# Performance work log

Measured on AMD Instinct MI355X. Metric: run time of the kernel, lower is better.

## Reference

```python
import jax, jax.numpy as jnp
import numpy as np

N = 100000       # num nodes
E = 3200000      # num edges (avg degree 32)
F_IN = 128       # num_node_features
HID = 16         # hidden dim hard-coded in Net
C = 10           # num_classes


def setup_inputs() -> dict:
    key = jax.random.key(0)
    k1, k2, k3, k4 = jax.random.split(key, 4)
    x = jax.random.normal(k1, (N, F_IN), dtype=jnp.float32)
    edge_index = jax.random.randint(k2, (2, E), 0, N, dtype=jnp.int32)
    W1 = jax.random.normal(k3, (F_IN, HID), dtype=jnp.float32) * 0.05
    b1 = jnp.zeros((HID,), dtype=jnp.float32)
    W2 = jax.random.normal(k4, (HID, C), dtype=jnp.float32) * 0.05
    b2 = jnp.zeros((C,), dtype=jnp.float32)
    return {"x": x, "edge_index": edge_index, "W1": W1, "b1": b1, "W2": W2, "b2": b2}


def reference(x, edge_index, W1, b1, W2, b2):
    # GCNConv: out = D^{-1/2} (A + I) D^{-1/2} X W + b   (add self-loops)
    loops = jnp.arange(N, dtype=edge_index.dtype)
    row = jnp.concatenate([edge_index[0], loops])  # source nodes
    col = jnp.concatenate([edge_index[1], loops])  # target nodes

    # symmetric normalization (degrees include self-loops, so deg >= 1)
    deg = jax.ops.segment_sum(jnp.ones_like(col, dtype=jnp.float32), col, num_segments=N)
    dis = jax.lax.rsqrt(deg)
    norm = dis[row] * dis[col]  # [E+N]

    def gcn_conv(h, W, b):
        h = h @ W                               # [N, d_out] small GEMM first
        msg = h[row] * norm[:, None]            # gather + scale, [E+N, d_out]
        out = jax.ops.segment_sum(msg, col, num_segments=N)  # scatter-add
        return out + b

    h = jax.nn.relu(gcn_conv(x, W1, b1))
    # F.dropout(training=False) is identity in eval mode
    logits = gcn_conv(h, W2, b2)
    return jax.nn.log_softmax(logits, axis=1)
```

## Files before the change

### kernel.cpp

```cpp
#include <hip/hip_runtime.h>
#include <math.h>

#define N_NODES 100000
#define N_EDGES 3200000
#define F_IN 128
#define HID 16
#define C_OUT 10
#define WIN 256
#define NDIG 391
#define PNB2 500
#define EPB 6400
#define SCN (NDIG * PNB2)
#define SB1 764
#define MAXE2 20
#define CSRLDS 10240

typedef unsigned short u16;
typedef unsigned int u32;

__device__ __forceinline__ float bf2f(u16 u) {
    return __uint_as_float(((u32)u) << 16);
}
__device__ __forceinline__ u16 f2bf(float f) {
    u32 x = __float_as_uint(f);
    u32 r = (x + 0x7fffu + ((x >> 16) & 1u)) >> 16;
    return (u16)r;
}
__device__ __forceinline__ void acc8(float* a, uint4 w) {
    a[0] += bf2f((u16)(w.x & 0xffff)); a[1] += bf2f((u16)(w.x >> 16));
    a[2] += bf2f((u16)(w.y & 0xffff)); a[3] += bf2f((u16)(w.y >> 16));
    a[4] += bf2f((u16)(w.z & 0xffff)); a[5] += bf2f((u16)(w.z >> 16));
    a[6] += bf2f((u16)(w.w & 0xffff)); a[7] += bf2f((u16)(w.w >> 16));
}

__global__ void k_pcnt(const int* __restrict__ col, int* __restrict__ blkhistA) {
    __shared__ int h[NDIG];
    for (int i = threadIdx.x; i < NDIG; i += 256) h[i] = 0;
    __syncthreads();
    const uint4* c4 = (const uint4*)(col + blockIdx.x * EPB);
    for (int i = threadIdx.x; i < EPB / 4; i += 256) {
        uint4 c = c4[i];
        atomicAdd(&h[c.x >> 8], 1);
        atomicAdd(&h[c.y >> 8], 1);
        atomicAdd(&h[c.z >> 8], 1);
        atomicAdd(&h[c.w >> 8], 1);
    }
    __syncthreads();
    for (int d = threadIdx.x; d < NDIG; d += 256)
        blkhistA[d * PNB2 + blockIdx.x] = h[d];
}

__global__ void k_s1(const int* __restrict__ blkhistA, int* __restrict__ psum) {
    __shared__ int sm[256];
    int i = blockIdx.x * 256 + threadIdx.x;
    sm[threadIdx.x] = (i < SCN) ? blkhistA[i] : 0;
    __syncthreads();
    for (int off = 128; off > 0; off >>= 1) {
        if (threadIdx.x < off) sm[threadIdx.x] += sm[threadIdx.x + off];
        __syncthreads();
    }
    if (threadIdx.x == 0) psum[blockIdx.x] = sm[0];
}

__global__ void k_s3(const int* __restrict__ blkhistA, const int* __restrict__ psum,
                     int* __restrict__ blkhistB) {
    __shared__ int ps[1024];
    __shared__ int sm[256];
    int t = threadIdx.x;
    for (int i = t; i < 1024; i += 256) ps[i] = (i < SB1) ? psum[i] : 0;
    __syncthreads();
    for (int off = 1; off < 1024; off <<= 1) {
        int v[4];
#pragma unroll
        for (int j = 0; j < 4; j++) {
            int idx = t + j * 256;
            v[j] = ps[idx] + ((idx >= off) ? ps[idx - off] : 0);
        }
        __syncthreads();
#pragma unroll
        for (int j = 0; j < 4; j++) ps[t + j * 256] = v[j];
        __syncthreads();
    }
    int bpre = (blockIdx.x > 0) ? ps[blockIdx.x - 1] : 0;

    int i = blockIdx.x * 256 + t;
    int v = (i < SCN) ? blkhistA[i] : 0;
    sm[t] = v;
    __syncthreads();
    for (int off = 1; off < 256; off <<= 1) {
        int a = sm[t];
        int b = (t >= off) ? sm[t - off] : 0;
        __syncthreads();
        sm[t] = a + b;
        __syncthreads();
    }
    if (i < SCN) blkhistB[i] = bpre + sm[t] - v;
}

__global__ void __launch_bounds__(512) k_pwrite(
        const int* __restrict__ row, const int* __restrict__ col,
        const int* __restrict__ blkhistA, const int* __restrict__ blkhistB,
        u32* __restrict__ staging) {
    __shared__ u32 sorted[EPB];
    __shared__ u16 dwin[EPB];
    __shared__ int gbase[NDIG];
    __shared__ int lbase[NDIG];
    __shared__ int lcur[NDIG];
    __shared__ int scan[512];

    int t = threadIdx.x;
    int b = blockIdx.x;
    int hv = 0;
    if (t < NDIG) {
        hv = blkhistA[t * PNB2 + b];
        gbase[t] = blkhistB[t * PNB2 + b];
        lcur[t] = 0;
    }
    scan[t] = hv;
    __syncthreads();
    for (int off = 1; off < 512; off <<= 1) {
        int v = scan[t];
        int u = (t >= off) ? scan[t - off] : 0;
        __syncthreads();
        scan[t] = v + u;
        __syncthreads();
    }
    if (t < NDIG) lbase[t] = scan[t] - hv;
    __syncthreads();

    const uint4* c4 = (const uint4*)(col + b * EPB);
    const uint4* r4 = (const uint4*)(row + b * EPB);
    for (int i = t; i < EPB / 4; i += 512) {
        uint4 c = c4[i];
        uint4 r = r4[i];
        int d, rank, pos;
        d = (int)(c.x >> 8); rank = atomicAdd(&lcur[d], 1); pos = lbase[d] + rank;
        sorted[pos] = ((c.x & 255u) << 17) | r.x; dwin[pos] = (u16)d;
        d = (int)(c.y >> 8); rank = atomicAdd(&lcur[d], 1); pos = lbase[d] + rank;
        sorted[pos] = ((c.y & 255u) << 17) | r.y; dwin[pos] = (u16)d;
        d = (int)(c.z >> 8); rank = atomicAdd(&lcur[d], 1); pos = lbase[d] + rank;
        sorted[pos] = ((c.z & 255u) << 17) | r.z; dwin[pos] = (u16)d;
        d = (int)(c.w >> 8); rank = atomicAdd(&lcur[d], 1); pos = lbase[d] + rank;
        sorted[pos] = ((c.w & 255u) << 17) | r.w; dwin[pos] = (u16)d;
    }
    __syncthreads();

    for (int i = t; i < EPB; i += 512) {
        int d = dwin[i];
        staging[gbase[d] + (i - lbase[d])] = sorted[i];
    }
}

__global__ void __launch_bounds__(512) k_csr(
        u32* staging, const int* __restrict__ blkhistB,
        int* __restrict__ offs, float* __restrict__ dis) {
    __shared__ u32 sorted[CSRLDS];
    __shared__ int cnt[WIN];
    __shared__ int base[WIN];
    int w = blockIdx.x;
    int t = threadIdx.x;
    if (t < WIN) cnt[t] = 0;
    __syncthreads();
    int start = blkhistB[w * PNB2];
    int end = (w == NDIG - 1) ? N_EDGES : blkhistB[(w + 1) * PNB2];
    int m = end - start;
    u32 buf[MAXE2];
    int n = 0;
#pragma unroll
    for (int k = 0; k < MAXE2; k++) {
        int i = k * 512 + t;
        if (i < m) {
            u32 e = staging[start + i];
            buf[k] = e;
            n = k + 1;
            atomicAdd(&cnt[e >> 17], 1);
        }
    }
    __syncthreads();
    if (t < WIN) base[t] = cnt[t];
    __syncthreads();
    for (int off = 1; off < WIN; off <<= 1) {
        int v = 0;
        if (t < WIN) {
            v = base[t];
            if (t >= off) v += base[t - off];
        }
        __syncthreads();
        if (t < WIN) base[t] = v;
        __syncthreads();
    }
    if (t < WIN) {
        int excl = base[t] - cnt[t];
        base[t] = excl;
        int node = w * WIN + t;
        if (node < N_NODES) {
            offs[node] = start + excl;
            dis[node] = rsqrtf(1.0f + (float)cnt[t]);
        }
    }
    if (w == 0 && t == 0) offs[N_NODES] = N_EDGES;
    __syncthreads();
#pragma unroll
    for (int k = 0; k < MAXE2; k++) {
        if (k < n) {
            u32 e = buf[k];
            int pos = atomicAdd(&base[(int)(e >> 17)], 1);
            sorted[pos] = e;
        }
    }
    __syncthreads();
    for (int i = t; i < m; i += 512)
        staging[start + i] = sorted[i];
}

__global__ void k_gemm1(const float* __restrict__ x, const float* __restrict__ W1,
                        const float* __restrict__ dis, u16* __restrict__ h1s) {
    __shared__ float Ws[F_IN * HID];
    for (int t = threadIdx.x; t < F_IN * HID; t += blockDim.x) Ws[t] = W1[t];
    __syncthreads();

    int node = blockIdx.x * blockDim.x + threadIdx.x;
    if (node >= N_NODES) return;

    float acc[HID];
#pragma unroll
    for (int j = 0; j < HID; j++) acc[j] = 0.f;

    const float4* xr = (const float4*)(x + (size_t)node * F_IN);
#pragma unroll 2
    for (int k4 = 0; k4 < F_IN / 4; k4++) {
        float4 v = xr[k4];
        float xv[4] = {v.x, v.y, v.z, v.w};
#pragma unroll
        for (int kk = 0; kk < 4; kk++) {
            const float4* wr = (const float4*)(Ws + (k4 * 4 + kk) * HID);
            float4 w0 = wr[0], w1 = wr[1], w2 = wr[2], w3 = wr[3];
            float xs = xv[kk];
            acc[0]  += xs * w0.x; acc[1]  += xs * w0.y; acc[2]  += xs * w0.z; acc[3]  += xs * w0.w;
            acc[4]  += xs * w1.x; acc[5]  += xs * w1.y; acc[6]  += xs * w1.z; acc[7]  += xs * w1.w;
            acc[8]  += xs * w2.x; acc[9]  += xs * w2.y; acc[10] += xs * w2.z; acc[11] += xs * w2.w;
            acc[12] += xs * w3.x; acc[13] += xs * w3.y; acc[14] += xs * w3.z; acc[15] += xs * w3.w;
        }
    }

    float d = dis[node];
    u32 p[8];
#pragma unroll
    for (int i = 0; i < 8; i++)
        p[i] = (u32)f2bf(acc[2 * i] * d) | ((u32)f2bf(acc[2 * i + 1] * d) << 16);
    u32* dst = (u32*)(h1s + (size_t)node * HID);
#pragma unroll
    for (int i = 0; i < 8; i++) dst[i] = p[i];
}

__global__ void k_gl1(const int* __restrict__ offs, const u32* __restrict__ csr,
                      const float* __restrict__ dis, const u16* __restrict__ h1s,
                      const float* __restrict__ b1, const float* __restrict__ W2,
                      u16* __restrict__ h2s) {
    __shared__ float Ws[HID * C_OUT];
    __shared__ float b1s[HID];
    if (threadIdx.x < HID * C_OUT) Ws[threadIdx.x] = W2[threadIdx.x];
    if (threadIdx.x < HID) b1s[threadIdx.x] = b1[threadIdx.x];
    __syncthreads();

    int t = blockIdx.x * 256 + threadIdx.x;
    if (t >= N_NODES * 8) return;
    int node = t >> 3;
    int q = t & 7;
    int half = q >> 2;
    int eq = q & 3;
    const uint4* hb = (const uint4*)h1s;
    float a[8] = {0.f, 0.f, 0.f, 0.f, 0.f, 0.f, 0.f, 0.f};
    if (eq == 0) acc8(a, hb[(size_t)node * 2 + half]);
    int o = offs[node + half];
    int oo = __shfl_xor(o, 4);
    int s0 = half ? oo : o;
    int s1 = half ? o : oo;
    int len = s1 - s0;
    int lo = s0 + ((len * eq) >> 2);
    int hi = s0 + ((len * (eq + 1)) >> 2);
    int j = lo;
    for (; j < hi && (j & 3); j++)
        acc8(a, hb[(size_t)(csr[j] & 0x1FFFFu) * 2 + half]);
    for (; j + 4 <= hi; j += 4) {
        uint4 ss = *(const uint4*)(csr + j);
        uint4 w0 = hb[(size_t)(ss.x & 0x1FFFFu) * 2 + half];
        uint4 w1 = hb[(size_t)(ss.y & 0x1FFFFu) * 2 + half];
        uint4 w2 = hb[(size_t)(ss.z & 0x1FFFFu) * 2 + half];
        uint4 w3 = hb[(size_t)(ss.w & 0x1FFFFu) * 2 + half];
        acc8(a, w0); acc8(a, w1); acc8(a, w2); acc8(a, w3);
    }
    for (; j < hi; j++)
        acc8(a, hb[(size_t)(csr[j] & 0x1FFFFu) * 2 + half]);

#pragma unroll
    for (int k = 0; k < 8; k++) {
        a[k] += __shfl_xor(a[k], 1);
        a[k] += __shfl_xor(a[k], 2);
    }

    float dc = dis[node];
    float own[8], oth[8];
#pragma unroll
    for (int k = 0; k < 8; k++) own[k] = a[k] * dc;
#pragma unroll
    for (int k = 0; k < 8; k++) oth[k] = __shfl_xor(own[k], 4);
    float h[16];
#pragma unroll
    for (int k = 0; k < 8; k++) {
        h[k]     = half ? oth[k] : own[k];
        h[8 + k] = half ? own[k] : oth[k];
    }
#pragma unroll
    for (int jj = 0; jj < 16; jj++) h[jj] = fmaxf(h[jj] + b1s[jj], 0.f);

    int nf = half ? 2 : 8;
    float outv[8];
#pragma unroll
    for (int k = 0; k < 8; k++) {
        float s = 0.f;
        if (k < nf) {
            int kk = half * 8 + k;
#pragma unroll
            for (int jj = 0; jj < 16; jj++) s += h[jj] * Ws[jj * C_OUT + kk];
        }
        outv[k] = s * dc;
    }
    if (eq == 0) {
        uint4 ov;
        ov.x = (u32)f2bf(outv[0]) | ((u32)f2bf(outv[1]) << 16);
        ov.y = half ? 0u : ((u32)f2bf(outv[2]) | ((u32)f2bf(outv[3]) << 16));
        ov.z = half ? 0u : ((u32)f2bf(outv[4]) | ((u32)f2bf(outv[5]) << 16));
        ov.w = half ? 0u : ((u32)f2bf(outv[6]) | ((u32)f2bf(outv[7]) << 16));
        ((uint4*)h2s)[(size_t)node * 2 + half] = ov;
    }
}

__global__ void k_gather2(const int* __restrict__ offs, const u32* __restrict__ csr,
                          const float* __restrict__ dis, const u16* __restrict__ h2s,
                          const float* __restrict__ b2, float* __restrict__ out) {
    __shared__ float b2s[C_OUT];
    if (threadIdx.x < C_OUT) b2s[threadIdx.x] = b2[threadIdx.x];
    __syncthreads();

    int t = blockIdx.x * 256 + threadIdx.x;
    if (t >= N_NODES * 8) return;
    int node = t >> 3;
    int q = t & 7;
    int half = q >> 2;
    int eq = q & 3;
    const uint4* hb = (const uint4*)h2s;
    float a[8] = {0.f, 0.f, 0.f, 0.f, 0.f, 0.f, 0.f, 0.f};
    if (eq == 0) acc8(a, hb[(size_t)node * 2 + half]);
    int o = offs[node + half];
    int oo = __shfl_xor(o, 4);
    int s0 = half ? oo : o;
    int s1 = half ? o : oo;
    int len = s1 - s0;
    int lo = s0 + ((len * eq) >> 2);
    int hi = s0 + ((len * (eq + 1)) >> 2);
    int j = lo;
    for (; j < hi && (j & 3); j++)
        acc8(a, hb[(size_t)(csr[j] & 0x1FFFFu) * 2 + half]);
    for (; j + 4 <= hi; j += 4) {
        uint4 ss = *(const uint4*)(csr + j);
        uint4 w0 = hb[(size_t)(ss.x & 0x1FFFFu) * 2 + half];
        uint4 w1 = hb[(size_t)(ss.y & 0x1FFFFu) * 2 + half];
        uint4 w2 = hb[(size_t)(ss.z & 0x1FFFFu) * 2 + half];
        uint4 w3 = hb[(size_t)(ss.w & 0x1FFFFu) * 2 + half];
        acc8(a, w0); acc8(a, w1); acc8(a, w2); acc8(a, w3);
    }
    for (; j < hi; j++)
        acc8(a, hb[(size_t)(csr[j] & 0x1FFFFu) * 2 + half]);

#pragma unroll
    for (int k = 0; k < 8; k++) {
        a[k] += __shfl_xor(a[k], 1);
        a[k] += __shfl_xor(a[k], 2);
    }

    float dc = dis[node];
    int nf = half ? 2 : 8;
    float lg[8];
    float m = -1e30f;
#pragma unroll
    for (int k = 0; k < 8; k++) {
        lg[k] = a[k] * dc + b2s[(half * 8 + k) % C_OUT];
        if (k < nf) m = fmaxf(m, lg[k]);
    }
    m = fmaxf(m, __shfl_xor(m, 4));
    float s = 0.f;
#pragma unroll
    for (int k = 0; k < 8; k++)
        if (k < nf) s += expf(lg[k] - m);
    s += __shfl_xor(s, 4);
    float ls = logf(s) + m;
    if (eq == 0) {
        float* dst = out + (size_t)node * C_OUT + half * 8;
        if (half == 0) {
#pragma unroll
            for (int i = 0; i < 4; i++)
                *(float2*)(dst + 2 * i) = make_float2(lg[2 * i] - ls, lg[2 * i + 1] - ls);
        } else {
            *(float2*)dst = make_float2(lg[0] - ls, lg[1] - ls);
        }
    }
}

extern "C" void kernel_launch(void* const* d_in, const int* in_sizes, int n_in,
                              void* d_out, int out_size, void* d_ws, size_t ws_size,
                              hipStream_t stream) {
    const float* x  = (const float*)d_in[0];
    const int*   ei = (const int*)d_in[1];
    const float* W1 = (const float*)d_in[2];
    const float* b1 = (const float*)d_in[3];
    const float* W2 = (const float*)d_in[4];
    const float* b2 = (const float*)d_in[5];
    float* out = (float*)d_out;

    const int* row = ei;
    const int* col = ei + N_EDGES;

    char* ws = (char*)d_ws;
    float* dis      = (float*)(ws);
    int*   offs     = (int*)(ws + 400000);
    int*   blkhistA = (int*)(ws + 800016);
    int*   blkhistB = (int*)(ws + 1582352);
    int*   psum     = (int*)(ws + 2364688);
    u32*   staging  = (u32*)(ws + 2367744);
    u16*   h1s      = (u16*)(ws + 15167744);
    u16*   h2s      = (u16*)(ws + 18367744);

    const int B = 256;
    int gN  = (N_NODES + B - 1) / B;
    int gN8 = (N_NODES * 8 + B - 1) / B;

    k_pcnt  <<<PNB2, B, 0, stream>>>(col, blkhistA);
    k_s1    <<<SB1, B, 0, stream>>>(blkhistA, psum);
    k_s3    <<<SB1, B, 0, stream>>>(blkhistA, psum, blkhistB);
    k_pwrite<<<PNB2, 512, 0, stream>>>(row, col, blkhistA, blkhistB, staging);
    k_csr   <<<NDIG, 512, 0, stream>>>(staging, blkhistB, offs, dis);
    k_gemm1 <<<gN, B, 0, stream>>>(x, W1, dis, h1s);
    k_gl1   <<<gN8, B, 0, stream>>>(offs, staging, dis, h1s, b1, W2, h2s);
    k_gather2<<<gN8, B, 0, stream>>>(offs, staging, dis, h2s, b2, out);
}
```

Baseline: 212.2 us.

## Sort nodes by degree within each window to balance gather warps

The CSR kernel now builds a per-window degree histogram and a counting sort that stores a permuted (node, degree) slot list plus per-slot edge start offsets. This replaces the offs array. Both gather kernels iterate over slots, so the threads in a wavefront handle nodes of similar degree, which should cut load imbalance and divergence. The gather inner loop is also unrolled to 8 edges to keep more loads in flight. Degree is stored in 8 bits and capped at 255, so the result would be wrong for any node with more than 255 in-edges.

```diff
diff --git a/kernel.cpp b/kernel.cpp
--- a/kernel.cpp
+++ b/kernel.cpp
@@ -14,6 +14,7 @@
 #define SB1 764
 #define MAXE2 20
 #define CSRLDS 10240
+#define NSLOT (NDIG * WIN)
 
 typedef unsigned short u16;
 typedef unsigned int u32;
@@ -153,13 +154,16 @@
 
 __global__ void __launch_bounds__(512) k_csr(
         u32* staging, const int* __restrict__ blkhistB,
-        int* __restrict__ offs, float* __restrict__ dis) {
+        u16* __restrict__ permdeg, int* __restrict__ starts, float* __restrict__ dis) {
     __shared__ u32 sorted[CSRLDS];
     __shared__ int cnt[WIN];
     __shared__ int base[WIN];
+    __shared__ int dh[256];
+    __shared__ int dsc[256];
     int w = blockIdx.x;
     int t = threadIdx.x;
     if (t < WIN) cnt[t] = 0;
+    if (t < 256) dh[t] = 0;
     __syncthreads();
     int start = blkhistB[w * PNB2];
     int end = (w == NDIG - 1) ? N_EDGES : blkhistB[(w + 1) * PNB2];
@@ -189,16 +193,44 @@
         if (t < WIN) base[t] = v;
         __syncthreads();
     }
+    int deg = 0, excl = 0;
+    int node = w * WIN + t;
     if (t < WIN) {
-        int excl = base[t] - cnt[t];
+        excl = base[t] - cnt[t];
         base[t] = excl;
-        int node = w * WIN + t;
+        deg = cnt[t];
         if (node < N_NODES) {
-            offs[node] = start + excl;
-            dis[node] = rsqrtf(1.0f + (float)cnt[t]);
-        }
-    }
-    if (w == 0 && t == 0) offs[N_NODES] = N_EDGES;
+            dis[node] = rsqrtf(1.0f + (float)deg);
+            atomicAdd(&dh[deg < 255 ? deg : 255], 1);
+        }
+    }
+    __syncthreads();
+    if (t < 256) dsc[t] = dh[t];
+    __syncthreads();
+    for (int off = 1; off < 256; off <<= 1) {
+        int v = 0;
+        if (t < 256) {
+            v = dsc[t];
+            if (t >= off) v += dsc[t - off];
+        }
+        __syncthreads();
+        if (t < 256) dsc[t] = v;
+        __syncthreads();
+    }
+    if (t < 256) dh[t] = dsc[t] - dh[t];
+    __syncthreads();
+    if (t < WIN) {
+        int rank, dcap = deg < 255 ? deg : 255;
+        if (node < N_NODES) {
+            rank = atomicAdd(&dh[dcap], 1);
+        } else {
+            rank = t;
+            dcap = 0;
+        }
+        int slot = w * WIN + rank;
+        permdeg[slot] = (u16)(t | (dcap << 8));
+        starts[slot] = start + excl;
+    }
     __syncthreads();
 #pragma unroll
     for (int k = 0; k < MAXE2; k++) {
@@ -253,8 +285,9 @@
     for (int i = 0; i < 8; i++) dst[i] = p[i];
 }
 
-__global__ void k_gl1(const int* __restrict__ offs, const u32* __restrict__ csr,
-                      const float* __restrict__ dis, const u16* __restrict__ h1s,
+__global__ void k_gl1(const u16* __restrict__ permdeg, const int* __restrict__ starts,
+                      const u32* __restrict__ csr, const float* __restrict__ dis,
+                      const u16* __restrict__ h1s,
                       const float* __restrict__ b1, const float* __restrict__ W2,
                       u16* __restrict__ h2s) {
     __shared__ float Ws[HID * C_OUT];
@@ -264,24 +297,37 @@
     __syncthreads();
 
     int t = blockIdx.x * 256 + threadIdx.x;
-    if (t >= N_NODES * 8) return;
-    int node = t >> 3;
+    int slot = t >> 3;
     int q = t & 7;
     int half = q >> 2;
     int eq = q & 3;
+    u32 pd = permdeg[slot];
+    int node = ((slot >> 8) << 8) + (int)(pd & 255u);
+    if (node >= N_NODES) return;
+    int deg = (int)(pd >> 8);
+    int s0 = starts[slot];
     const uint4* hb = (const uint4*)h1s;
     float a[8] = {0.f, 0.f, 0.f, 0.f, 0.f, 0.f, 0.f, 0.f};
     if (eq == 0) acc8(a, hb[(size_t)node * 2 + half]);
-    int o = offs[node + half];
-    int oo = __shfl_xor(o, 4);
-    int s0 = half ? oo : o;
-    int s1 = half ? o : oo;
-    int len = s1 - s0;
-    int lo = s0 + ((len * eq) >> 2);
-    int hi = s0 + ((len * (eq + 1)) >> 2);
+    int lo = s0 + ((deg * eq) >> 2);
+    int hi = s0 + ((deg * (eq + 1)) >> 2);
     int j = lo;
     for (; j < hi && (j & 3); j++)
         acc8(a, hb[(size_t)(csr[j] & 0x1FFFFu) * 2 + half]);
+    for (; j + 8 <= hi; j += 8) {
+        uint4 sa = *(const uint4*)(csr + j);
+        uint4 sb = *(const uint4*)(csr + j + 4);
+        uint4 w0 = hb[(size_t)(sa.x & 0x1FFFFu) * 2 + half];
+        uint4 w1 = hb[(size_t)(sa.y & 0x1FFFFu) * 2 + half];
+        uint4 w2 = hb[(size_t)(sa.z & 0x1FFFFu) * 2 + half];
+        uint4 w3 = hb[(size_t)(sa.w & 0x1FFFFu) * 2 + half];
+        uint4 w4 = hb[(size_t)(sb.x & 0x1FFFFu) * 2 + half];
+        uint4 w5 = hb[(size_t)(sb.y & 0x1FFFFu) * 2 + half];
+        uint4 w6 = hb[(size_t)(sb.z & 0x1FFFFu) * 2 + half];
+        uint4 w7 = hb[(size_t)(sb.w & 0x1FFFFu) * 2 + half];
+        acc8(a, w0); acc8(a, w1); acc8(a, w2); acc8(a, w3);
+        acc8(a, w4); acc8(a, w5); acc8(a, w6); acc8(a, w7);
+    }
     for (; j + 4 <= hi; j += 4) {
         uint4 ss = *(const uint4*)(csr + j);
         uint4 w0 = hb[(size_t)(ss.x & 0x1FFFFu) * 2 + half];
@@ -336,32 +382,46 @@
     }
 }
 
-__global__ void k_gather2(const int* __restrict__ offs, const u32* __restrict__ csr,
-                          const float* __restrict__ dis, const u16* __restrict__ h2s,
+__global__ void k_gather2(const u16* __restrict__ permdeg, const int* __restrict__ starts,
+                          const u32* __restrict__ csr, const float* __restrict__ dis,
+                          const u16* __restrict__ h2s,
                           const float* __restrict__ b2, float* __restrict__ out) {
     __shared__ float b2s[C_OUT];
     if (threadIdx.x < C_OUT) b2s[threadIdx.x] = b2[threadIdx.x];
     __syncthreads();
 
     int t = blockIdx.x * 256 + threadIdx.x;
-    if (t >= N_NODES * 8) return;
-    int node = t >> 3;
+    int slot = t >> 3;
     int q = t & 7;
     int half = q >> 2;
     int eq = q & 3;
+    u32 pd = permdeg[slot];
+    int node = ((slot >> 8) << 8) + (int)(pd & 255u);
+    if (node >= N_NODES) return;
+    int deg = (int)(pd >> 8);
+    int s0 = starts[slot];
     const uint4* hb = (const uint4*)h2s;
     float a[8] = {0.f, 0.f, 0.f, 0.f, 0.f, 0.f, 0.f, 0.f};
     if (eq == 0) acc8(a, hb[(size_t)node * 2 + half]);
-    int o = offs[node + half];
-    int oo = __shfl_xor(o, 4);
-    int s0 = half ? oo : o;
-    int s1 = half ? o : oo;
-    int len = s1 - s0;
-    int lo = s0 + ((len * eq) >> 2);
-    int hi = s0 + ((len * (eq + 1)) >> 2);
+    int lo = s0 + ((deg * eq) >> 2);
+    int hi = s0 + ((deg * (eq + 1)) >> 2);
     int j = lo;
     for (; j < hi && (j & 3); j++)
         acc8(a, hb[(size_t)(csr[j] & 0x1FFFFu) * 2 + half]);
+    for (; j + 8 <= hi; j += 8) {
+        uint4 sa = *(const uint4*)(csr + j);
+        uint4 sb = *(const uint4*)(csr + j + 4);
+        uint4 w0 = hb[(size_t)(sa.x & 0x1FFFFu) * 2 + half];
+        uint4 w1 = hb[(size_t)(sa.y & 0x1FFFFu) * 2 + half];
+        uint4 w2 = hb[(size_t)(sa.z & 0x1FFFFu) * 2 + half];
+        uint4 w3 = hb[(size_t)(sa.w & 0x1FFFFu) * 2 + half];
+        uint4 w4 = hb[(size_t)(sb.x & 0x1FFFFu) * 2 + half];
+        uint4 w5 = hb[(size_t)(sb.y & 0x1FFFFu) * 2 + half];
+        uint4 w6 = hb[(size_t)(sb.z & 0x1FFFFu) * 2 + half];
+        uint4 w7 = hb[(size_t)(sb.w & 0x1FFFFu) * 2 + half];
+        acc8(a, w0); acc8(a, w1); acc8(a, w2); acc8(a, w3);
+        acc8(a, w4); acc8(a, w5); acc8(a, w6); acc8(a, w7);
+    }
     for (; j + 4 <= hi; j += 4) {
         uint4 ss = *(const uint4*)(csr + j);
         uint4 w0 = hb[(size_t)(ss.x & 0x1FFFFu) * 2 + half];
@@ -423,24 +483,25 @@
 
     char* ws = (char*)d_ws;
     float* dis      = (float*)(ws);
-    int*   offs     = (int*)(ws + 400000);
-    int*   blkhistA = (int*)(ws + 800016);
-    int*   blkhistB = (int*)(ws + 1582352);
-    int*   psum     = (int*)(ws + 2364688);
-    u32*   staging  = (u32*)(ws + 2367744);
-    u16*   h1s      = (u16*)(ws + 15167744);
-    u16*   h2s      = (u16*)(ws + 18367744);
+    int*   blkhistA = (int*)(ws + 400000);
+    int*   blkhistB = (int*)(ws + 1182336);
+    int*   psum     = (int*)(ws + 1964672);
+    u16*   permdeg  = (u16*)(ws + 400000);
+    int*   starts   = (int*)(ws + 600192);
+    u32*   staging  = (u32*)(ws + 1967744);
+    u16*   h1s      = (u16*)(ws + 14767744);
+    u16*   h2s      = (u16*)(ws + 17967744);
 
     const int B = 256;
     int gN  = (N_NODES + B - 1) / B;
-    int gN8 = (N_NODES * 8 + B - 1) / B;
+    int gS8 = (NSLOT * 8) / B;
 
     k_pcnt  <<<PNB2, B, 0, stream>>>(col, blkhistA);
     k_s1    <<<SB1, B, 0, stream>>>(blkhistA, psum);
     k_s3    <<<SB1, B, 0, stream>>>(blkhistA, psum, blkhistB);
     k_pwrite<<<PNB2, 512, 0, stream>>>(row, col, blkhistA, blkhistB, staging);
-    k_csr   <<<NDIG, 512, 0, stream>>>(staging, blkhistB, offs, dis);
+    k_csr   <<<NDIG, 512, 0, stream>>>(staging, blkhistB, permdeg, starts, dis);
     k_gemm1 <<<gN, B, 0, stream>>>(x, W1, dis, h1s);
-    k_gl1   <<<gN8, B, 0, stream>>>(offs, staging, dis, h1s, b1, W2, h2s);
-    k_gather2<<<gN8, B, 0, stream>>>(offs, staging, dis, h2s, b2, out);
-}
+    k_gl1   <<<gS8, B, 0, stream>>>(permdeg, starts, staging, dis, h1s, b1, W2, h2s);
+    k_gather2<<<gS8, B, 0, stream>>>(permdeg, starts, staging, dis, h2s, b2, out);
+}
```

New measurement: 232.8 us. +9.7%, slower.

## Fuse CSR window sort into layer-1 gather, reading edges from LDS

Applied to the files above, without the earlier changes.

Splits the old CSR kernel into a lightweight degree-count kernel (for dis, needed by gemm1) and moves the per-window counting sort into the layer-1 gather kernel. That kernel now gathers neighbour features using the sorted edge list held in shared memory instead of re-reading CSR from global memory, and computes the normalisation from the local count. The aim is to remove a global write/read round trip of the edge list and one launch. The cost is an extra pass over staging to count degrees, and only 391 blocks of 512 threads for the gather, which limits occupancy and latency hiding. The layer-2 gather also gains an 8-wide unrolled loop for more loads in flight.

```diff
diff --git a/kernel.cpp b/kernel.cpp
--- a/kernel.cpp
+++ b/kernel.cpp
@@ -151,66 +151,22 @@
     }
 }
 
-__global__ void __launch_bounds__(512) k_csr(
-        u32* staging, const int* __restrict__ blkhistB,
-        int* __restrict__ offs, float* __restrict__ dis) {
-    __shared__ u32 sorted[CSRLDS];
+__global__ void __launch_bounds__(512) k_deg(
+        const u32* __restrict__ staging, const int* __restrict__ blkhistB,
+        float* __restrict__ dis) {
     __shared__ int cnt[WIN];
-    __shared__ int base[WIN];
     int w = blockIdx.x;
     int t = threadIdx.x;
     if (t < WIN) cnt[t] = 0;
     __syncthreads();
     int start = blkhistB[w * PNB2];
     int end = (w == NDIG - 1) ? N_EDGES : blkhistB[(w + 1) * PNB2];
-    int m = end - start;
-    u32 buf[MAXE2];
-    int n = 0;
-#pragma unroll
-    for (int k = 0; k < MAXE2; k++) {
-        int i = k * 512 + t;
-        if (i < m) {
-            u32 e = staging[start + i];
-            buf[k] = e;
-            n = k + 1;
-            atomicAdd(&cnt[e >> 17], 1);
-        }
-    }
-    __syncthreads();
-    if (t < WIN) base[t] = cnt[t];
-    __syncthreads();
-    for (int off = 1; off < WIN; off <<= 1) {
-        int v = 0;
-        if (t < WIN) {
-            v = base[t];
-            if (t >= off) v += base[t - off];
-        }
-        __syncthreads();
-        if (t < WIN) base[t] = v;
-        __syncthreads();
-    }
-    if (t < WIN) {
-        int excl = base[t] - cnt[t];
-        base[t] = excl;
-        int node = w * WIN + t;
-        if (node < N_NODES) {
-            offs[node] = start + excl;
-            dis[node] = rsqrtf(1.0f + (float)cnt[t]);
-        }
-    }
-    if (w == 0 && t == 0) offs[N_NODES] = N_EDGES;
-    __syncthreads();
-#pragma unroll
-    for (int k = 0; k < MAXE2; k++) {
-        if (k < n) {
-            u32 e = buf[k];
-            int pos = atomicAdd(&base[(int)(e >> 17)], 1);
-            sorted[pos] = e;
-        }
-    }
-    __syncthreads();
-    for (int i = t; i < m; i += 512)
-        staging[start + i] = sorted[i];
+    for (int i = start + t; i < end; i += 512)
+        atomicAdd(&cnt[staging[i] >> 17], 1);
+    __syncthreads();
+    int node = w * WIN + t;
+    if (t < WIN && node < N_NODES)
+        dis[node] = rsqrtf(1.0f + (float)cnt[t]);
 }
 
 __global__ void k_gemm1(const float* __restrict__ x, const float* __restrict__ W1,
@@ -253,86 +209,139 @@
     for (int i = 0; i < 8; i++) dst[i] = p[i];
 }
 
-__global__ void k_gl1(const int* __restrict__ offs, const u32* __restrict__ csr,
-                      const float* __restrict__ dis, const u16* __restrict__ h1s,
-                      const float* __restrict__ b1, const float* __restrict__ W2,
-                      u16* __restrict__ h2s) {
+__global__ void __launch_bounds__(512) k_gl1f(
+        u32* staging, const int* __restrict__ blkhistB,
+        const u16* __restrict__ h1s, const float* __restrict__ b1,
+        const float* __restrict__ W2,
+        int* __restrict__ offs, u16* __restrict__ h2s) {
+    __shared__ u32 sorted[CSRLDS];
+    __shared__ int cnt[WIN];
+    __shared__ int sbase[WIN];
+    __shared__ int cur[WIN];
     __shared__ float Ws[HID * C_OUT];
     __shared__ float b1s[HID];
-    if (threadIdx.x < HID * C_OUT) Ws[threadIdx.x] = W2[threadIdx.x];
-    if (threadIdx.x < HID) b1s[threadIdx.x] = b1[threadIdx.x];
-    __syncthreads();
-
-    int t = blockIdx.x * 256 + threadIdx.x;
-    if (t >= N_NODES * 8) return;
-    int node = t >> 3;
-    int q = t & 7;
-    int half = q >> 2;
-    int eq = q & 3;
+    int w = blockIdx.x;
+    int t = threadIdx.x;
+    if (t < HID * C_OUT) Ws[t] = W2[t];
+    if (t < HID) b1s[t] = b1[t];
+    if (t < WIN) cnt[t] = 0;
+    __syncthreads();
+    int start = blkhistB[w * PNB2];
+    int end = (w == NDIG - 1) ? N_EDGES : blkhistB[(w + 1) * PNB2];
+    int m = end - start;
+    u32 buf[MAXE2];
+    int n = 0;
+#pragma unroll
+    for (int k = 0; k < MAXE2; k++) {
+        int i = k * 512 + t;
+        if (i < m) {
+            u32 e = staging[start + i];
+            buf[k] = e;
+            n = k + 1;
+            atomicAdd(&cnt[e >> 17], 1);
+        }
+    }
+    __syncthreads();
+    if (t < WIN) sbase[t] = cnt[t];
+    __syncthreads();
+    for (int off = 1; off < WIN; off <<= 1) {
+        int v = 0;
+        if (t < WIN) {
+            v = sbase[t];
+            if (t >= off) v += sbase[t - off];
+        }
+        __syncthreads();
+        if (t < WIN) sbase[t] = v;
+        __syncthreads();
+    }
+    if (t < WIN) {
+        int excl = sbase[t] - cnt[t];
+        sbase[t] = excl;
+        cur[t] = excl;
+        int node = w * WIN + t;
+        if (node < N_NODES) offs[node] = start + excl;
+    }
+    if (w == 0 && t == 0) offs[N_NODES] = N_EDGES;
+    __syncthreads();
+#pragma unroll
+    for (int k = 0; k < MAXE2; k++) {
+        if (k < n) {
+            u32 e = buf[k];
+            int pos = atomicAdd(&cur[(int)(e >> 17)], 1);
+            sorted[pos] = e;
+        }
+    }
+    __syncthreads();
+    for (int i = t; i < m; i += 512)
+        staging[start + i] = sorted[i];
+
     const uint4* hb = (const uint4*)h1s;
-    float a[8] = {0.f, 0.f, 0.f, 0.f, 0.f, 0.f, 0.f, 0.f};
-    if (eq == 0) acc8(a, hb[(size_t)node * 2 + half]);
-    int o = offs[node + half];
-    int oo = __shfl_xor(o, 4);
-    int s0 = half ? oo : o;
-    int s1 = half ? o : oo;
-    int len = s1 - s0;
-    int lo = s0 + ((len * eq) >> 2);
-    int hi = s0 + ((len * (eq + 1)) >> 2);
-    int j = lo;
-    for (; j < hi && (j & 3); j++)
-        acc8(a, hb[(size_t)(csr[j] & 0x1FFFFu) * 2 + half]);
-    for (; j + 4 <= hi; j += 4) {
-        uint4 ss = *(const uint4*)(csr + j);
-        uint4 w0 = hb[(size_t)(ss.x & 0x1FFFFu) * 2 + half];
-        uint4 w1 = hb[(size_t)(ss.y & 0x1FFFFu) * 2 + half];
-        uint4 w2 = hb[(size_t)(ss.z & 0x1FFFFu) * 2 + half];
-        uint4 w3 = hb[(size_t)(ss.w & 0x1FFFFu) * 2 + half];
-        acc8(a, w0); acc8(a, w1); acc8(a, w2); acc8(a, w3);
-    }
-    for (; j < hi; j++)
-        acc8(a, hb[(size_t)(csr[j] & 0x1FFFFu) * 2 + half]);
-
-#pragma unroll
-    for (int k = 0; k < 8; k++) {
-        a[k] += __shfl_xor(a[k], 1);
-        a[k] += __shfl_xor(a[k], 2);
-    }
-
-    float dc = dis[node];
-    float own[8], oth[8];
-#pragma unroll
-    for (int k = 0; k < 8; k++) own[k] = a[k] * dc;
-#pragma unroll
-    for (int k = 0; k < 8; k++) oth[k] = __shfl_xor(own[k], 4);
-    float h[16];
-#pragma unroll
-    for (int k = 0; k < 8; k++) {
-        h[k]     = half ? oth[k] : own[k];
-        h[8 + k] = half ? own[k] : oth[k];
-    }
-#pragma unroll
-    for (int jj = 0; jj < 16; jj++) h[jj] = fmaxf(h[jj] + b1s[jj], 0.f);
-
-    int nf = half ? 2 : 8;
-    float outv[8];
-#pragma unroll
-    for (int k = 0; k < 8; k++) {
-        float s = 0.f;
-        if (k < nf) {
-            int kk = half * 8 + k;
-#pragma unroll
-            for (int jj = 0; jj < 16; jj++) s += h[jj] * Ws[jj * C_OUT + kk];
-        }
-        outv[k] = s * dc;
-    }
-    if (eq == 0) {
-        uint4 ov;
-        ov.x = (u32)f2bf(outv[0]) | ((u32)f2bf(outv[1]) << 16);
-        ov.y = half ? 0u : ((u32)f2bf(outv[2]) | ((u32)f2bf(outv[3]) << 16));
-        ov.z = half ? 0u : ((u32)f2bf(outv[4]) | ((u32)f2bf(outv[5]) << 16));
-        ov.w = half ? 0u : ((u32)f2bf(outv[6]) | ((u32)f2bf(outv[7]) << 16));
-        ((uint4*)h2s)[(size_t)node * 2 + half] = ov;
+    int half = (t >> 2) & 1;
+    int eq = t & 3;
+#pragma unroll 1
+    for (int rep = 0; rep < 4; rep++) {
+        int nl = rep * 64 + (t >> 3);
+        int node = w * WIN + nl;
+        bool valid = node < N_NODES;
+        float a[8] = {0.f, 0.f, 0.f, 0.f, 0.f, 0.f, 0.f, 0.f};
+        int deg = valid ? cnt[nl] : 0;
+        int s0 = sbase[nl];
+        if (valid && eq == 0) acc8(a, hb[(size_t)node * 2 + half]);
+        int lo = s0 + ((deg * eq) >> 2);
+        int hi = s0 + ((deg * (eq + 1)) >> 2);
+        int j = lo;
+        for (; j + 4 <= hi; j += 4) {
+            u32 e0 = sorted[j], e1 = sorted[j + 1], e2 = sorted[j + 2], e3 = sorted[j + 3];
+            uint4 w0 = hb[(size_t)(e0 & 0x1FFFFu) * 2 + half];
+            uint4 w1 = hb[(size_t)(e1 & 0x1FFFFu) * 2 + half];
+            uint4 w2 = hb[(size_t)(e2 & 0x1FFFFu) * 2 + half];
+            uint4 w3 = hb[(size_t)(e3 & 0x1FFFFu) * 2 + half];
+            acc8(a, w0); acc8(a, w1); acc8(a, w2); acc8(a, w3);
+        }
+        for (; j < hi; j++)
+            acc8(a, hb[(size_t)(sorted[j] & 0x1FFFFu) * 2 + half]);
+
+#pragma unroll
+        for (int k = 0; k < 8; k++) {
+            a[k] += __shfl_xor(a[k], 1);
+            a[k] += __shfl_xor(a[k], 2);
+        }
+
+        float dc = rsqrtf(1.0f + (float)deg);
+        float own[8], oth[8];
+#pragma unroll
+        for (int k = 0; k < 8; k++) own[k] = a[k] * dc;
+#pragma unroll
+        for (int k = 0; k < 8; k++) oth[k] = __shfl_xor(own[k], 4);
+        float h[16];
+#pragma unroll
+        for (int k = 0; k < 8; k++) {
+            h[k]     = half ? oth[k] : own[k];
+            h[8 + k] = half ? own[k] : oth[k];
+        }
+#pragma unroll
+        for (int jj = 0; jj < 16; jj++) h[jj] = fmaxf(h[jj] + b1s[jj], 0.f);
+
+        int nf = half ? 2 : 8;
+        float outv[8];
+#pragma unroll
+        for (int k = 0; k < 8; k++) {
+            float s = 0.f;
+            if (k < nf) {
+                int kk = half * 8 + k;
+#pragma unroll
+                for (int jj = 0; jj < 16; jj++) s += h[jj] * Ws[jj * C_OUT + kk];
+            }
+            outv[k] = s * dc;
+        }
+        if (valid && eq == 0) {
+            uint4 ov;
+            ov.x = (u32)f2bf(outv[0]) | ((u32)f2bf(outv[1]) << 16);
+            ov.y = half ? 0u : ((u32)f2bf(outv[2]) | ((u32)f2bf(outv[3]) << 16));
+            ov.z = half ? 0u : ((u32)f2bf(outv[4]) | ((u32)f2bf(outv[5]) << 16));
+            ov.w = half ? 0u : ((u32)f2bf(outv[6]) | ((u32)f2bf(outv[7]) << 16));
+            ((uint4*)h2s)[(size_t)node * 2 + half] = ov;
+        }
     }
 }
 
@@ -362,6 +371,20 @@
     int j = lo;
     for (; j < hi && (j & 3); j++)
         acc8(a, hb[(size_t)(csr[j] & 0x1FFFFu) * 2 + half]);
+    for (; j + 8 <= hi; j += 8) {
+        uint4 sa = *(const uint4*)(csr + j);
+        uint4 sb = *(const uint4*)(csr + j + 4);
+        uint4 w0 = hb[(size_t)(sa.x & 0x1FFFFu) * 2 + half];
+        uint4 w1 = hb[(size_t)(sa.y & 0x1FFFFu) * 2 + half];
+        uint4 w2 = hb[(size_t)(sa.z & 0x1FFFFu) * 2 + half];
+        uint4 w3 = hb[(size_t)(sa.w & 0x1FFFFu) * 2 + half];
+        uint4 w4 = hb[(size_t)(sb.x & 0x1FFFFu) * 2 + half];
+        uint4 w5 = hb[(size_t)(sb.y & 0x1FFFFu) * 2 + half];
+        uint4 w6 = hb[(size_t)(sb.z & 0x1FFFFu) * 2 + half];
+        uint4 w7 = hb[(size_t)(sb.w & 0x1FFFFu) * 2 + half];
+        acc8(a, w0); acc8(a, w1); acc8(a, w2); acc8(a, w3);
+        acc8(a, w4); acc8(a, w5); acc8(a, w6); acc8(a, w7);
+    }
     for (; j + 4 <= hi; j += 4) {
         uint4 ss = *(const uint4*)(csr + j);
         uint4 w0 = hb[(size_t)(ss.x & 0x1FFFFu) * 2 + half];
@@ -439,8 +462,8 @@
     k_s1    <<<SB1, B, 0, stream>>>(blkhistA, psum);
     k_s3    <<<SB1, B, 0, stream>>>(blkhistA, psum, blkhistB);
     k_pwrite<<<PNB2, 512, 0, stream>>>(row, col, blkhistA, blkhistB, staging);
-    k_csr   <<<NDIG, 512, 0, stream>>>(staging, blkhistB, offs, dis);
+    k_deg   <<<NDIG, 512, 0, stream>>>(staging, blkhistB, dis);
     k_gemm1 <<<gN, B, 0, stream>>>(x, W1, dis, h1s);
-    k_gl1   <<<gN8, B, 0, stream>>>(offs, staging, dis, h1s, b1, W2, h2s);
+    k_gl1f  <<<NDIG, 512, 0, stream>>>(staging, blkhistB, h1s, b1, W2, offs, h2s);
     k_gather2<<<gN8, B, 0, stream>>>(offs, staging, dis, h2s, b2, out);
 }
```

Measured after the change: 212.2 us. No clear change (+0.0%).
